# Optimization experiments

Hardware: AMD Instinct MI355X
Metric: run time of the kernel (lower is better)

## Reference

```python
import jax, jax.numpy as jnp
import numpy as np

N = 100000   # nodes
E = 1600000  # edges (avg degree 16)
F = 256      # in_channels
H = 4        # heads
C = 32       # out_channels per head
NEG_SLOPE = 0.2  # PyG GATConv default leaky_relu slope


def setup_inputs() -> dict:
    key = jax.random.key(0)
    k0, k1, k2, k3, k4 = jax.random.split(key, 5)
    x = jax.random.normal(k0, (N, F), dtype=jnp.float32)
    edge_index = jax.random.randint(k1, (2, E), 0, N, dtype=jnp.int32)
    W = jax.random.normal(k2, (F, H * C), dtype=jnp.float32) * 0.05
    att_src = jax.random.normal(k3, (H, C), dtype=jnp.float32) * 0.05
    att_dst = jax.random.normal(k4, (H, C), dtype=jnp.float32) * 0.05
    bias = jnp.zeros((H * C,), dtype=jnp.float32)
    return {"x": x, "edge_index": edge_index, "W": W,
            "att_src": att_src, "att_dst": att_dst, "bias": bias}


def reference(x, edge_index, W, att_src, att_dst, bias):
    n = x.shape[0]
    h_, c_ = att_src.shape
    # add self loops (PyG default add_self_loops=True)
    loops = jnp.arange(n, dtype=edge_index.dtype)
    src = jnp.concatenate([edge_index[0], loops])  # source node j of each edge
    dst = jnp.concatenate([edge_index[1], loops])  # target node i of each edge
    # linear projection, per-head view: [N, H, C]
    h = (x @ W).reshape(n, h_, c_)
    # per-node attention halves: [N, H]
    a_src = jnp.einsum('nhc,hc->nh', h, att_src)
    a_dst = jnp.einsum('nhc,hc->nh', h, att_dst)
    # per-edge logits with leaky relu: [Etot, H]
    e = jax.nn.leaky_relu(a_src[src] + a_dst[dst], NEG_SLOPE)
    # segment softmax over edges sharing the same destination
    m = jax.ops.segment_max(e, dst, num_segments=n)
    m = jnp.where(jnp.isfinite(m), m, jnp.zeros_like(m))  # isolated nodes
    p = jnp.exp(e - m[dst])
    s = jax.ops.segment_sum(p, dst, num_segments=n)
    alpha = p / (s[dst] + 1e-16)  # [Etot, H]
    # weighted scatter-aggregate of source features
    msg = h[src] * alpha[:, :, None]  # [Etot, H, C]
    out = jax.ops.segment_sum(msg, dst, num_segments=n)  # [N, H, C]
    return out.reshape(n, h_ * c_) + bias
```

## Files before the change

kernel.cpp:

```cpp
#include <hip/hip_runtime.h>

#define NEG_SLOPE 0.2f
#define CAP 64
#define NPART 8

typedef __attribute__((ext_vector_type(8))) short short8;
typedef __attribute__((ext_vector_type(4))) float f32x4;

__device__ __forceinline__ float lrelu(float x) {
    return x > 0.0f ? x : NEG_SLOPE * x;
}

__device__ __forceinline__ unsigned short f2bf(float f) {
    unsigned int u = __float_as_uint(f);
    u += 0x7FFFu + ((u >> 16) & 1u);
    return (unsigned short)(u >> 16);
}

__device__ __forceinline__ float2 bfpair(unsigned int u) {
    float2 r;
    r.x = __uint_as_float(u << 16);
    r.y = __uint_as_float(u & 0xFFFF0000u);
    return r;
}

__global__ void convW_kernel(const float* __restrict__ W, unsigned short* __restrict__ Wt) {
    int idx = blockIdx.x * blockDim.x + threadIdx.x;
    int nn = idx & 127;
    int kk = idx >> 7;
    Wt[nn * 256 + kk] = f2bf(W[kk * 128 + nn]);
}

__global__ __launch_bounds__(256) void gemm_fused_kernel(
    const float* __restrict__ x, const unsigned short* __restrict__ Wt,
    const float* __restrict__ att_src, const float* __restrict__ att_dst,
    unsigned short* __restrict__ hb, float* __restrict__ a_src,
    float* __restrict__ a_dst, int n) {
    int wave = threadIdx.x >> 6;
    int lane = threadIdx.x & 63;
    int ln = lane & 15;
    int quad = lane >> 4;
    int row0 = blockIdx.x * 64 + wave * 16;

    int arow = row0 + ln;
    if (arow >= n) arow = n - 1;
    const float* xrow = &x[(size_t)arow * 256];

    f32x4 acc[8];
    #pragma unroll
    for (int t = 0; t < 8; ++t) acc[t] = (f32x4){0.f, 0.f, 0.f, 0.f};

    #pragma unroll
    for (int ks = 0; ks < 8; ++ks) {
        int k0 = ks * 32;
        float4 a0 = *(const float4*)&xrow[k0 + quad * 8];
        float4 a1 = *(const float4*)&xrow[k0 + quad * 8 + 4];
        short8 afrag;
        afrag[0] = (short)f2bf(a0.x); afrag[1] = (short)f2bf(a0.y);
        afrag[2] = (short)f2bf(a0.z); afrag[3] = (short)f2bf(a0.w);
        afrag[4] = (short)f2bf(a1.x); afrag[5] = (short)f2bf(a1.y);
        afrag[6] = (short)f2bf(a1.z); afrag[7] = (short)f2bf(a1.w);
        #pragma unroll
        for (int t = 0; t < 8; ++t) {
            short8 bfrag = *(const short8*)&Wt[(size_t)(t * 16 + ln) * 256 + k0 + quad * 8];
            acc[t] = __builtin_amdgcn_mfma_f32_16x16x32_bf16(afrag, bfrag, acc[t], 0, 0, 0);
        }
    }

    #pragma unroll
    for (int t = 0; t < 8; ++t) {
        #pragma unroll
        for (int r = 0; r < 4; ++r) {
            int grow = row0 + quad * 4 + r;
            if (grow < n) hb[(size_t)grow * 128 + t * 16 + ln] = f2bf(acc[t][r]);
        }
    }

    #pragma unroll
    for (int hd = 0; hd < 4; ++hd) {
        float as1 = att_src[hd * 32 + ln];
        float as2 = att_src[hd * 32 + 16 + ln];
        float ad1 = att_dst[hd * 32 + ln];
        float ad2 = att_dst[hd * 32 + 16 + ln];
        #pragma unroll
        for (int r = 0; r < 4; ++r) {
            float ps = acc[2 * hd][r] * as1 + acc[2 * hd + 1][r] * as2;
            float pd = acc[2 * hd][r] * ad1 + acc[2 * hd + 1][r] * ad2;
            #pragma unroll
            for (int off = 1; off < 16; off <<= 1) {
                ps += __shfl_xor(ps, off);
                pd += __shfl_xor(pd, off);
            }
            if (ln == 0) {
                int grow = row0 + quad * 4 + r;
                if (grow < n) {
                    a_src[grow * 4 + hd] = ps;
                    a_dst[grow * 4 + hd] = pd;
                }
            }
        }
    }
}

__global__ __launch_bounds__(256) void build_kernel(
    const int* __restrict__ src, const int* __restrict__ dst,
    int* __restrict__ deg, int* __restrict__ bucket, int e, int n) {
    int p = blockIdx.x & (NPART - 1);
    int slice = blockIdx.x >> 3;
    int nslices = gridDim.x >> 3;
    int part = (n + NPART - 1) / NPART;
    int lo = p * part;
    int hi = lo + part;
    int stride = nslices * 256;
    for (int i = slice * 256 + threadIdx.x; i < e; i += stride) {
        int d = dst[i];
        if (d >= lo && d < hi) {
            int r = atomicAdd(&deg[d], 1);
            if (r < CAP) bucket[(size_t)d * CAP + r] = src[i];
        }
    }
}

__global__ __launch_bounds__(256) void aggregate_kernel(
    const unsigned short* __restrict__ hb, const float* __restrict__ a_src,
    const float* __restrict__ a_dst, const int* __restrict__ deg,
    const int* __restrict__ bucket, const float* __restrict__ bias,
    float* __restrict__ out, int n) {
    int node = blockIdx.x * 4 + (threadIdx.x >> 6);
    if (node >= n) return;
    int lane = threadIdx.x & 63;
    int hh = lane >> 4;
    const unsigned int* hbu = (const unsigned int*)hb;
    const int* bkt = &bucket[(size_t)node * CAP];

    float adst = a_dst[node * 4 + hh];
    int cnt = deg[node];
    if (cnt > CAP) cnt = CAP;

    float m = lrelu(a_src[node * 4 + hh] + adst);
    float d = 1.0f;
    float2 acc = bfpair(hbu[(size_t)node * 64 + lane]);

    int p = 0;
    for (; p + 4 <= cnt; p += 4) {
        int4 s4 = *(const int4*)&bkt[p];
        unsigned int v0 = hbu[(size_t)s4.x * 64 + lane];
        unsigned int v1 = hbu[(size_t)s4.y * 64 + lane];
        unsigned int v2 = hbu[(size_t)s4.z * 64 + lane];
        unsigned int v3 = hbu[(size_t)s4.w * 64 + lane];
        float e0 = lrelu(a_src[s4.x * 4 + hh] + adst);
        float e1 = lrelu(a_src[s4.y * 4 + hh] + adst);
        float e2 = lrelu(a_src[s4.z * 4 + hh] + adst);
        float e3 = lrelu(a_src[s4.w * 4 + hh] + adst);
        float nm = fmaxf(fmaxf(fmaxf(e0, e1), fmaxf(e2, e3)), m);
        float sc = __expf(m - nm);
        float p0 = __expf(e0 - nm);
        float p1 = __expf(e1 - nm);
        float p2 = __expf(e2 - nm);
        float p3 = __expf(e3 - nm);
        m = nm;
        d = d * sc + p0 + p1 + p2 + p3;
        float2 h0 = bfpair(v0), h1 = bfpair(v1), h2 = bfpair(v2), h3 = bfpair(v3);
        acc.x = acc.x * sc + p0 * h0.x + p1 * h1.x + p2 * h2.x + p3 * h3.x;
        acc.y = acc.y * sc + p0 * h0.y + p1 * h1.y + p2 * h2.y + p3 * h3.y;
    }
    for (; p < cnt; ++p) {
        int s = bkt[p];
        unsigned int v = hbu[(size_t)s * 64 + lane];
        float ev = lrelu(a_src[s * 4 + hh] + adst);
        float nm = fmaxf(ev, m);
        float sc = __expf(m - nm);
        float pe = __expf(ev - nm);
        m = nm;
        d = d * sc + pe;
        float2 hv = bfpair(v);
        acc.x = acc.x * sc + pe * hv.x;
        acc.y = acc.y * sc + pe * hv.y;
    }

    float inv = 1.0f / d;
    int oc = hh * 32 + (lane & 15) * 2;
    float2 b2 = *(const float2*)&bias[oc];
    float2 o;
    o.x = acc.x * inv + b2.x;
    o.y = acc.y * inv + b2.y;
    *(float2*)&out[(size_t)node * 128 + oc] = o;
}

extern "C" void kernel_launch(void* const* d_in, const int* in_sizes, int n_in,
                              void* d_out, int out_size, void* d_ws, size_t ws_size,
                              hipStream_t stream) {
    const float* x = (const float*)d_in[0];
    const int* edge_index = (const int*)d_in[1];
    const float* W = (const float*)d_in[2];
    const float* att_src = (const float*)d_in[3];
    const float* att_dst = (const float*)d_in[4];
    const float* bias = (const float*)d_in[5];
    float* out = (float*)d_out;

    int n = in_sizes[0] / 256;
    int e = in_sizes[1] / 2;
    const int* esrc = edge_index;
    const int* edst = edge_index + e;

    char* w = (char*)d_ws;
    unsigned short* hb = (unsigned short*)w;  w += (size_t)n * 128 * 2;
    float* a_src = (float*)w;                 w += (size_t)n * 4 * 4;
    float* a_dst = (float*)w;                 w += (size_t)n * 4 * 4;
    unsigned short* Wt = (unsigned short*)w;  w += 128 * 256 * 2;
    int* deg = (int*)w;                       w += (size_t)n * 4;
    int* bucket = (int*)w;                    w += (size_t)n * CAP * 4;

    hipMemsetAsync(deg, 0, (size_t)n * sizeof(int), stream);

    convW_kernel<<<128, 256, 0, stream>>>(W, Wt);
    gemm_fused_kernel<<<(n + 63) / 64, 256, 0, stream>>>(x, Wt, att_src, att_dst,
                                                         hb, a_src, a_dst, n);
    build_kernel<<<256 * NPART, 256, 0, stream>>>(esrc, edst, deg, bucket, e, n);
    aggregate_kernel<<<(n + 3) / 4, 256, 0, stream>>>(hb, a_src, a_dst, deg,
                                                      bucket, bias, out, n);
}
```

Measured before the change: 389.4 us.

## Stage x in LDS, pre-swizzle W, vectorize bucket build, two-pass softmax aggregate

The GEMM now stages the x tile as bf16 in shared memory with coalesced float4 loads. W is pre-swizzled into MFMA fragment order, so each B fragment becomes one contiguous load. The build kernel reads edges as int4 and tests the partition with an unsigned range check. The aggregate kernel splits the online softmax into two passes: first it computes max, sum and alpha per neighbor with 16-lane reductions and writes them to LDS, then it does a plain weighted gather. This adds LDS use and a block barrier, and degrees above 64 are still truncated.

After: 377.6 us. -3.0%, faster.

```diff
diff --git a/kernel.cpp b/kernel.cpp
--- a/kernel.cpp
+++ b/kernel.cpp
@@ -24,27 +24,47 @@
     return r;
 }
 
-__global__ void convW_kernel(const float* __restrict__ W, unsigned short* __restrict__ Wt) {
+__global__ void convW_kernel(const float* __restrict__ W, unsigned short* __restrict__ Wtf) {
     int idx = blockIdx.x * blockDim.x + threadIdx.x;
-    int nn = idx & 127;
-    int kk = idx >> 7;
-    Wt[nn * 256 + kk] = f2bf(W[kk * 128 + nn]);
-}
-
+    int j = idx & 7;
+    int lane = (idx >> 3) & 63;
+    int f = idx >> 9;
+    int t = f >> 3;
+    int ks = f & 7;
+    int k = ks * 32 + (lane >> 4) * 8 + j;
+    int nn = t * 16 + (lane & 15);
+    Wtf[idx] = f2bf(W[k * 128 + nn]);
+}
+
+#define XS_STRIDE 280
 __global__ __launch_bounds__(256) void gemm_fused_kernel(
-    const float* __restrict__ x, const unsigned short* __restrict__ Wt,
+    const float* __restrict__ x, const unsigned short* __restrict__ Wtf,
     const float* __restrict__ att_src, const float* __restrict__ att_dst,
     unsigned short* __restrict__ hb, float* __restrict__ a_src,
     float* __restrict__ a_dst, int n) {
-    int wave = threadIdx.x >> 6;
-    int lane = threadIdx.x & 63;
+    __shared__ unsigned short xs[64 * XS_STRIDE];
+    int tid = threadIdx.x;
+    int row0 = blockIdx.x * 64;
+
+    #pragma unroll
+    for (int it = 0; it < 16; ++it) {
+        int flat = tid * 4 + it * 1024;
+        int r = flat >> 8;
+        int c = flat & 255;
+        int gr = row0 + r;
+        if (gr >= n) gr = n - 1;
+        float4 v = *(const float4*)&x[(size_t)gr * 256 + c];
+        unsigned short b0 = f2bf(v.x), b1 = f2bf(v.y), b2 = f2bf(v.z), b3 = f2bf(v.w);
+        unsigned short* dp = &xs[r * XS_STRIDE + c];
+        dp[0] = b0; dp[1] = b1; dp[2] = b2; dp[3] = b3;
+    }
+    __syncthreads();
+
+    int wave = tid >> 6;
+    int lane = tid & 63;
     int ln = lane & 15;
     int quad = lane >> 4;
-    int row0 = blockIdx.x * 64 + wave * 16;
-
-    int arow = row0 + ln;
-    if (arow >= n) arow = n - 1;
-    const float* xrow = &x[(size_t)arow * 256];
+    int row0w = row0 + wave * 16;
 
     f32x4 acc[8];
     #pragma unroll
@@ -52,17 +72,10 @@
 
     #pragma unroll
     for (int ks = 0; ks < 8; ++ks) {
-        int k0 = ks * 32;
-        float4 a0 = *(const float4*)&xrow[k0 + quad * 8];
-        float4 a1 = *(const float4*)&xrow[k0 + quad * 8 + 4];
-        short8 afrag;
-        afrag[0] = (short)f2bf(a0.x); afrag[1] = (short)f2bf(a0.y);
-        afrag[2] = (short)f2bf(a0.z); afrag[3] = (short)f2bf(a0.w);
-        afrag[4] = (short)f2bf(a1.x); afrag[5] = (short)f2bf(a1.y);
-        afrag[6] = (short)f2bf(a1.z); afrag[7] = (short)f2bf(a1.w);
+        short8 afrag = *(const short8*)&xs[(wave * 16 + ln) * XS_STRIDE + ks * 32 + quad * 8];
         #pragma unroll
         for (int t = 0; t < 8; ++t) {
-            short8 bfrag = *(const short8*)&Wt[(size_t)(t * 16 + ln) * 256 + k0 + quad * 8];
+            short8 bfrag = *(const short8*)&Wtf[(((t * 8 + ks) * 64) + lane) * 8];
             acc[t] = __builtin_amdgcn_mfma_f32_16x16x32_bf16(afrag, bfrag, acc[t], 0, 0, 0);
         }
     }
@@ -71,7 +84,7 @@
     for (int t = 0; t < 8; ++t) {
         #pragma unroll
         for (int r = 0; r < 4; ++r) {
-            int grow = row0 + quad * 4 + r;
+            int grow = row0w + quad * 4 + r;
             if (grow < n) hb[(size_t)grow * 128 + t * 16 + ln] = f2bf(acc[t][r]);
         }
     }
@@ -92,7 +105,7 @@
                 pd += __shfl_xor(pd, off);
             }
             if (ln == 0) {
-                int grow = row0 + quad * 4 + r;
+                int grow = row0w + quad * 4 + r;
                 if (grow < n) {
                     a_src[grow * 4 + hd] = ps;
                     a_dst[grow * 4 + hd] = pd;
@@ -109,15 +122,36 @@
     int slice = blockIdx.x >> 3;
     int nslices = gridDim.x >> 3;
     int part = (n + NPART - 1) / NPART;
-    int lo = p * part;
-    int hi = lo + part;
+    unsigned lo = (unsigned)(p * part);
+    int e4 = e >> 2;
     int stride = nslices * 256;
-    for (int i = slice * 256 + threadIdx.x; i < e; i += stride) {
+    const int4* dst4 = (const int4*)dst;
+    const int4* src4 = (const int4*)src;
+    for (int i = slice * 256 + threadIdx.x; i < e4; i += stride) {
+        int4 d4 = dst4[i];
+        int4 s4 = src4[i];
+        if ((unsigned)(d4.x - lo) < (unsigned)part) {
+            int r = atomicAdd(&deg[d4.x], 1);
+            if (r < CAP) bucket[d4.x * CAP + r] = s4.x;
+        }
+        if ((unsigned)(d4.y - lo) < (unsigned)part) {
+            int r = atomicAdd(&deg[d4.y], 1);
+            if (r < CAP) bucket[d4.y * CAP + r] = s4.y;
+        }
+        if ((unsigned)(d4.z - lo) < (unsigned)part) {
+            int r = atomicAdd(&deg[d4.z], 1);
+            if (r < CAP) bucket[d4.z * CAP + r] = s4.z;
+        }
+        if ((unsigned)(d4.w - lo) < (unsigned)part) {
+            int r = atomicAdd(&deg[d4.w], 1);
+            if (r < CAP) bucket[d4.w * CAP + r] = s4.w;
+        }
+    }
+    if (blockIdx.x == 0 && threadIdx.x < (e & 3)) {
+        int i = e4 * 4 + threadIdx.x;
         int d = dst[i];
-        if (d >= lo && d < hi) {
-            int r = atomicAdd(&deg[d], 1);
-            if (r < CAP) bucket[(size_t)d * CAP + r] = src[i];
-        }
+        int r = atomicAdd(&deg[d], 1);
+        if (r < CAP) bucket[d * CAP + r] = src[i];
     }
 }
 
@@ -126,64 +160,103 @@
     const float* __restrict__ a_dst, const int* __restrict__ deg,
     const int* __restrict__ bucket, const float* __restrict__ bias,
     float* __restrict__ out, int n) {
-    int node = blockIdx.x * 4 + (threadIdx.x >> 6);
-    if (node >= n) return;
+    __shared__ float lds_alpha[4][CAP][4];
+    __shared__ int lds_s[4][CAP];
+    int wave = threadIdx.x >> 6;
     int lane = threadIdx.x & 63;
+    int node = blockIdx.x * 4 + wave;
+    if (node >= n) node = n - 1;
+    int el = lane & 15;
     int hh = lane >> 4;
-    const unsigned int* hbu = (const unsigned int*)hb;
-    const int* bkt = &bucket[(size_t)node * CAP];
-
-    float adst = a_dst[node * 4 + hh];
+
     int cnt = deg[node];
     if (cnt > CAP) cnt = CAP;
 
-    float m = lrelu(a_src[node * 4 + hh] + adst);
-    float d = 1.0f;
-    float2 acc = bfpair(hbu[(size_t)node * 64 + lane]);
-
+    float adst = a_dst[node * 4 + hh];
+    float e_self = lrelu(a_src[node * 4 + hh] + adst);
+
+    float e_gp[4];
+    int s_gp[4];
+    float mloc = e_self;
+    #pragma unroll
+    for (int g = 0; g < 4; ++g) {
+        int p = g * 16 + el;
+        if (p < cnt) {
+            int s = bucket[node * CAP + p];
+            s_gp[g] = s;
+            float ev = lrelu(a_src[s * 4 + hh] + adst);
+            e_gp[g] = ev;
+            mloc = fmaxf(mloc, ev);
+        } else {
+            s_gp[g] = node;
+            e_gp[g] = -INFINITY;
+        }
+    }
+    #pragma unroll
+    for (int off = 1; off < 16; off <<= 1)
+        mloc = fmaxf(mloc, __shfl_xor(mloc, off));
+
+    float pe_gp[4];
+    float dloc = 0.0f;
+    #pragma unroll
+    for (int g = 0; g < 4; ++g) {
+        float pe = __expf(e_gp[g] - mloc);
+        pe_gp[g] = pe;
+        dloc += pe;
+    }
+    #pragma unroll
+    for (int off = 1; off < 16; off <<= 1)
+        dloc += __shfl_xor(dloc, off);
+
+    float pe_self = __expf(e_self - mloc);
+    float inv = 1.0f / (dloc + pe_self);
+    float alpha_self = pe_self * inv;
+
+    #pragma unroll
+    for (int g = 0; g < 4; ++g) {
+        lds_alpha[wave][g * 16 + el][hh] = pe_gp[g] * inv;
+        if (hh == 0) lds_s[wave][g * 16 + el] = s_gp[g];
+    }
+    __syncthreads();
+
+    const unsigned int* hbu = (const unsigned int*)hb;
+    float2 acc;
+    {
+        float2 hv = bfpair(hbu[(unsigned)node * 64u + lane]);
+        acc.x = alpha_self * hv.x;
+        acc.y = alpha_self * hv.y;
+    }
     int p = 0;
     for (; p + 4 <= cnt; p += 4) {
-        int4 s4 = *(const int4*)&bkt[p];
-        unsigned int v0 = hbu[(size_t)s4.x * 64 + lane];
-        unsigned int v1 = hbu[(size_t)s4.y * 64 + lane];
-        unsigned int v2 = hbu[(size_t)s4.z * 64 + lane];
-        unsigned int v3 = hbu[(size_t)s4.w * 64 + lane];
-        float e0 = lrelu(a_src[s4.x * 4 + hh] + adst);
-        float e1 = lrelu(a_src[s4.y * 4 + hh] + adst);
-        float e2 = lrelu(a_src[s4.z * 4 + hh] + adst);
-        float e3 = lrelu(a_src[s4.w * 4 + hh] + adst);
-        float nm = fmaxf(fmaxf(fmaxf(e0, e1), fmaxf(e2, e3)), m);
-        float sc = __expf(m - nm);
-        float p0 = __expf(e0 - nm);
-        float p1 = __expf(e1 - nm);
-        float p2 = __expf(e2 - nm);
-        float p3 = __expf(e3 - nm);
-        m = nm;
-        d = d * sc + p0 + p1 + p2 + p3;
+        int s0 = lds_s[wave][p + 0];
+        int s1 = lds_s[wave][p + 1];
+        int s2 = lds_s[wave][p + 2];
+        int s3 = lds_s[wave][p + 3];
+        float al0 = lds_alpha[wave][p + 0][hh];
+        float al1 = lds_alpha[wave][p + 1][hh];
+        float al2 = lds_alpha[wave][p + 2][hh];
+        float al3 = lds_alpha[wave][p + 3][hh];
+        unsigned int v0 = hbu[(unsigned)s0 * 64u + lane];
+        unsigned int v1 = hbu[(unsigned)s1 * 64u + lane];
+        unsigned int v2 = hbu[(unsigned)s2 * 64u + lane];
+        unsigned int v3 = hbu[(unsigned)s3 * 64u + lane];
         float2 h0 = bfpair(v0), h1 = bfpair(v1), h2 = bfpair(v2), h3 = bfpair(v3);
-        acc.x = acc.x * sc + p0 * h0.x + p1 * h1.x + p2 * h2.x + p3 * h3.x;
-        acc.y = acc.y * sc + p0 * h0.y + p1 * h1.y + p2 * h2.y + p3 * h3.y;
+        acc.x += al0 * h0.x + al1 * h1.x + al2 * h2.x + al3 * h3.x;
+        acc.y += al0 * h0.y + al1 * h1.y + al2 * h2.y + al3 * h3.y;
     }
     for (; p < cnt; ++p) {
-        int s = bkt[p];
-        unsigned int v = hbu[(size_t)s * 64 + lane];
-        float ev = lrelu(a_src[s * 4 + hh] + adst);
-        float nm = fmaxf(ev, m);
-        float sc = __expf(m - nm);
-        float pe = __expf(ev - nm);
-        m = nm;
-        d = d * sc + pe;
-        float2 hv = bfpair(v);
-        acc.x = acc.x * sc + pe * hv.x;
-        acc.y = acc.y * sc + pe * hv.y;
-    }
-
-    float inv = 1.0f / d;
-    int oc = hh * 32 + (lane & 15) * 2;
+        int s = lds_s[wave][p];
+        float al = lds_alpha[wave][p][hh];
+        float2 hv = bfpair(hbu[(unsigned)s * 64u + lane]);
+        acc.x += al * hv.x;
+        acc.y += al * hv.y;
+    }
+
+    int oc = hh * 32 + el * 2;
     float2 b2 = *(const float2*)&bias[oc];
     float2 o;
-    o.x = acc.x * inv + b2.x;
-    o.y = acc.y * inv + b2.y;
+    o.x = acc.x + b2.x;
+    o.y = acc.y + b2.y;
     *(float2*)&out[(size_t)node * 128 + oc] = o;
 }
 
@@ -207,14 +280,14 @@
     unsigned short* hb = (unsigned short*)w;  w += (size_t)n * 128 * 2;
     float* a_src = (float*)w;                 w += (size_t)n * 4 * 4;
     float* a_dst = (float*)w;                 w += (size_t)n * 4 * 4;
-    unsigned short* Wt = (unsigned short*)w;  w += 128 * 256 * 2;
+    unsigned short* Wtf = (unsigned short*)w; w += 128 * 256 * 2;
     int* deg = (int*)w;                       w += (size_t)n * 4;
     int* bucket = (int*)w;                    w += (size_t)n * CAP * 4;
 
     hipMemsetAsync(deg, 0, (size_t)n * sizeof(int), stream);
 
-    convW_kernel<<<128, 256, 0, stream>>>(W, Wt);
-    gemm_fused_kernel<<<(n + 63) / 64, 256, 0, stream>>>(x, Wt, att_src, att_dst,
+    convW_kernel<<<128, 256, 0, stream>>>(W, Wtf);
+    gemm_fused_kernel<<<(n + 63) / 64, 256, 0, stream>>>(x, Wtf, att_src, att_dst,
                                                          hb, a_src, a_dst, n);
     build_kernel<<<256 * NPART, 256, 0, stream>>>(esrc, edst, deg, bucket, e, n);
     aggregate_kernel<<<(n + 3) / 4, 256, 0, stream>>>(hb, a_src, a_dst, deg,
```
